# Optimization experiments

Hardware: AMD Instinct MI355X
Metric: run time of the kernel (lower is better)

The kernel has to match this reference:

```python
import jax, jax.numpy as jnp
import numpy as np

N = 50000      # nodes
E = 800000     # directed edges
GNN_DIM = 128  # node feature dim
HID = 64       # per-head hidden dim of conv1
HEADS = 2
OUT = 16       # output_dim (classes)
TEXT = 500     # tf-idf text dim
M = 10000      # masked / labeled nodes


def setup_inputs() -> dict:
    key = jax.random.key(0)
    ks = jax.random.split(key, 32)
    w = lambda k, s: jax.random.normal(k, s, jnp.float32) * 0.05
    inp = {
        'text_features': jax.random.normal(ks[0], (M, TEXT), jnp.float32),
        'x': jax.random.normal(ks[1], (N, GNN_DIM), jnp.float32),
        'edge_index': jax.random.randint(ks[2], (2, E), 0, N),
        'mask': jax.random.randint(ks[3], (M,), 0, N),
        # text MLP (Linear stored as [in, out])
        'fc1_w': w(ks[4], (TEXT, 128)), 'fc1_b': w(ks[5], (128,)),
        'fc2_w': w(ks[6], (128, 64)),  'fc2_b': w(ks[7], (64,)),
        'fc3_w': w(ks[8], (64, 16)),   'fc3_b': w(ks[9], (16,)),
        'fc4_w': w(ks[10], (16, OUT)), 'fc4_b': w(ks[11], (OUT,)),
        'sc_w': w(ks[12], (TEXT, OUT)), 'sc_b': w(ks[13], (OUT,)),
        # GATConv1: in=GNN_DIM, heads=2, out=HID, concat=True
        'W1': w(ks[14], (GNN_DIM, HEADS * HID)),
        'att_src1': w(ks[15], (HEADS, HID)), 'att_dst1': w(ks[16], (HEADS, HID)),
        'b1': w(ks[17], (HEADS * HID,)),
        # GATConv2: in=2*HID, heads=1, out=OUT, concat=False
        'W2': w(ks[18], (HEADS * HID, OUT)),
        'att_src2': w(ks[19], (1, OUT)), 'att_dst2': w(ks[20], (1, OUT)),
        'b2': w(ks[21], (OUT,)),
        # fc_final: [2*OUT, OUT]
        'fcf_w': w(ks[22], (2 * OUT, OUT)), 'fcf_b': w(ks[23], (OUT,)),
    }
    return inp


def _gat_layer(h_in, src, dst, W, a_src, a_dst, b, heads, dim, concat):
    # PyG GATConv (default negative_slope=0.2, self-loops already appended)
    n = h_in.shape[0]
    h = (h_in @ W).reshape(n, heads, dim)                      # [N,H,D]
    a_s = jnp.einsum('nhd,hd->nh', h, a_src)                   # [N,H]
    a_d = jnp.einsum('nhd,hd->nh', h, a_dst)
    e = jax.nn.leaky_relu(a_s[src] + a_d[dst], 0.2)            # [E,H]
    emax = jax.ops.segment_max(e, dst, num_segments=n)
    ex = jnp.exp(e - emax[dst])
    den = jax.ops.segment_sum(ex, dst, num_segments=n)
    alpha = ex / (den[dst] + 1e-16)                            # [E,H]
    msg = h[src] * alpha[:, :, None]                           # [E,H,D]
    out = jax.ops.segment_sum(msg, dst, num_segments=n)        # [N,H,D]
    out = out.reshape(n, heads * dim) if concat else out.mean(axis=1)
    return out + b


def reference(text_features, x, edge_index, mask,
              fc1_w, fc1_b, fc2_w, fc2_b, fc3_w, fc3_b, fc4_w, fc4_b,
              sc_w, sc_b, W1, att_src1, att_dst1, b1,
              W2, att_src2, att_dst2, b2, fcf_w, fcf_b):
    n = x.shape[0]
    loop = jnp.arange(n, dtype=edge_index.dtype)
    src = jnp.concatenate([edge_index[0], loop])
    dst = jnp.concatenate([edge_index[1], loop])

    # GNN branch
    g = jax.nn.relu(_gat_layer(x, src, dst, W1, att_src1, att_dst1, b1,
                               HEADS, HID, True))
    g = _gat_layer(g, src, dst, W2, att_src2, att_dst2, b2, 1, OUT, False)
    gnn_out = g[mask]                                          # [M,OUT]

    # text MLP branch with shortcut
    t = jax.nn.relu(text_features @ fc1_w + fc1_b)
    t = jax.nn.relu(t @ fc2_w + fc2_b)
    t = jax.nn.relu(t @ fc3_w + fc3_b)
    text_out = (t @ fc4_w + fc4_b) + (text_features @ sc_w + sc_b)  # [M,OUT]

    combined = jnp.concatenate([text_out, gnn_out], axis=1)    # [M,2*OUT]
    return jax.nn.log_softmax(combined @ fcf_w + fcf_b, axis=1)
```

## Files before the change

### kernel.cpp

```cpp
#include <hip/hip_runtime.h>
#include <hip/hip_bf16.h>
#include <cmath>

#define TEXTD 500
#define GNN_DIM 128
#define DEGP(v) ((v) << 5)

typedef __attribute__((ext_vector_type(8))) short bf16x8;
typedef __attribute__((ext_vector_type(4))) float f32x4;

__device__ __forceinline__ float bf2f(unsigned short u) {
    union { unsigned int i; float f; } cv;
    cv.i = ((unsigned int)u) << 16;
    return cv.f;
}
__device__ __forceinline__ unsigned short f2b(float x) {
    __hip_bfloat16 b = __float2bfloat16(x);
    return *reinterpret_cast<unsigned short*>(&b);
}
__device__ __forceinline__ float u2f(unsigned int u) {
    union { unsigned int i; float f; } cv; cv.i = u; return cv.f;
}
__device__ __forceinline__ bf16x8 cvt8(const float* p) {
    float4 u = *(const float4*)p;
    float4 v = *(const float4*)(p + 4);
    bf16x8 f;
    f[0] = (short)f2b(u.x); f[1] = (short)f2b(u.y);
    f[2] = (short)f2b(u.z); f[3] = (short)f2b(u.w);
    f[4] = (short)f2b(v.x); f[5] = (short)f2b(v.y);
    f[6] = (short)f2b(v.z); f[7] = (short)f2b(v.w);
    return f;
}

__global__ __launch_bounds__(256) void setup_kernel(
    int* __restrict__ deg, int N, int NB,
    const float* __restrict__ fc1_w, const float* __restrict__ sc_w,
    const float* __restrict__ W1, const float* __restrict__ W2,
    const float* __restrict__ fc2_w, const float* __restrict__ fc3_w,
    const float* __restrict__ fc4_w,
    unsigned short* __restrict__ w1cat, unsigned short* __restrict__ w1g,
    unsigned short* __restrict__ w2t, unsigned short* __restrict__ fc2t,
    unsigned short* __restrict__ fc3t, unsigned short* __restrict__ fc4t)
{
    if ((int)blockIdx.x < NB) {
        int v = blockIdx.x * 256 + threadIdx.x;
        if (v < N) deg[DEGP(v)] = 0;
        return;
    }
    int idx = (blockIdx.x - NB) * 256 + threadIdx.x;
    if (idx < 73728) {
        int n = idx >> 9, k = idx & 511;
        float v = 0.f;
        if (k < TEXTD) v = (n < 128) ? fc1_w[k * 128 + n] : sc_w[k * 16 + (n - 128)];
        w1cat[idx] = f2b(v);
    } else if (idx < 90112) {
        int j = idx - 73728;
        int n = j >> 7, k = j & 127;
        w1g[j] = f2b(W1[k * 128 + n]);
    } else if (idx < 92160) {
        int j = idx - 90112;
        int n = j >> 7, k = j & 127;
        w2t[j] = f2b(W2[k * 16 + n]);
    } else if (idx < 100352) {
        int j = idx - 92160;
        int n = j >> 7, k = j & 127;
        fc2t[j] = f2b(fc2_w[k * 64 + n]);
    } else if (idx < 101376) {
        int j = idx - 100352;
        int n = j >> 6, k = j & 63;
        fc3t[j] = f2b(fc3_w[k * 16 + n]);
    } else if (idx < 101888) {
        int j = idx - 101376;
        int n = j >> 5, k = j & 31;
        fc4t[j] = f2b((k < 16) ? fc4_w[k * 16 + n] : 0.f);
    }
}

__global__ __launch_bounds__(256) void text_mfma_kernel(
    const float* __restrict__ text, const short* __restrict__ w1cat,
    const float* __restrict__ fc1_b, const float* __restrict__ sc_b,
    const short* __restrict__ fc2t, const float* __restrict__ fc2_b,
    const short* __restrict__ fc3t, const float* __restrict__ fc3_b,
    const short* __restrict__ fc4t, const float* __restrict__ fc4_b,
    float* __restrict__ text_out, int M)
{
    __shared__ float part[4 * 9 * 256];
    __shared__ unsigned short t1b[16 * 136];
    __shared__ unsigned short t2b[16 * 72];
    __shared__ unsigned short t3b[16 * 40];
    __shared__ float tscs[16 * 16];

    const int tid = threadIdx.x;
    const int w = tid >> 6, lane = tid & 63;
    const int q = lane >> 4, col = lane & 15;
    const int mb = blockIdx.x * 16;
    const int arow = min(mb + col, M - 1);
    const int kofs = w * 128;

    bf16x8 afrag[4];
    #pragma unroll
    for (int ks = 0; ks < 4; ks++) {
        int k0 = kofs + ks * 32 + q * 8;
        if (k0 + 7 < TEXTD) {
            afrag[ks] = cvt8(text + (size_t)arow * TEXTD + k0);
        } else {
            bf16x8 f;
            #pragma unroll
            for (int e = 0; e < 8; e++) {
                int k = k0 + e;
                f[e] = (short)((k < TEXTD) ? f2b(text[(size_t)arow * TEXTD + k]) : 0);
            }
            afrag[ks] = f;
        }
    }

    for (int nb = 0; nb < 9; nb++) {
        const short* bp = w1cat + (size_t)(nb * 16 + col) * 512 + kofs + q * 8;
        f32x4 acc = {0.f, 0.f, 0.f, 0.f};
        #pragma unroll
        for (int ks = 0; ks < 4; ks++)
            acc = __builtin_amdgcn_mfma_f32_16x16x32_bf16(afrag[ks], *(const bf16x8*)(bp + ks * 32), acc, 0, 0, 0);
        #pragma unroll
        for (int i = 0; i < 4; i++)
            part[w * 2304 + nb * 256 + i * 64 + lane] = acc[i];
    }
    __syncthreads();

    {
        int nb0 = w * 2;
        int cnt = (w == 3) ? 3 : 2;
        for (int t = 0; t < cnt; t++) {
            int nb = nb0 + t;
            #pragma unroll
            for (int i = 0; i < 4; i++) {
                float a = part[nb * 256 + i * 64 + lane]
                        + part[2304 + nb * 256 + i * 64 + lane]
                        + part[4608 + nb * 256 + i * 64 + lane]
                        + part[6912 + nb * 256 + i * 64 + lane];
                int row = q * 4 + i;
                if (nb < 8) t1b[row * 136 + nb * 16 + col] = f2b(fmaxf(a + fc1_b[nb * 16 + col], 0.f));
                else        tscs[row * 16 + col] = a + sc_b[col];
            }
        }
    }
    __syncthreads();

    {
        const unsigned short* a2p = t1b + col * 136 + q * 8;
        const short* bp = fc2t + (w * 16 + col) * 128 + q * 8;
        f32x4 acc = {0.f, 0.f, 0.f, 0.f};
        #pragma unroll
        for (int ks = 0; ks < 4; ks++)
            acc = __builtin_amdgcn_mfma_f32_16x16x32_bf16(
                *(const bf16x8*)(a2p + ks * 32), *(const bf16x8*)(bp + ks * 32), acc, 0, 0, 0);
        #pragma unroll
        for (int i = 0; i < 4; i++) {
            int row = q * 4 + i;
            t2b[row * 72 + w * 16 + col] = f2b(fmaxf(acc[i] + fc2_b[w * 16 + col], 0.f));
        }
    }
    __syncthreads();

    if (w == 0) {
        {
            const unsigned short* a3p = t2b + col * 72 + q * 8;
            const short* bp = fc3t + col * 64 + q * 8;
            f32x4 acc = {0.f, 0.f, 0.f, 0.f};
            #pragma unroll
            for (int ks = 0; ks < 2; ks++)
                acc = __builtin_amdgcn_mfma_f32_16x16x32_bf16(
                    *(const bf16x8*)(a3p + ks * 32), *(const bf16x8*)(bp + ks * 32), acc, 0, 0, 0);
            #pragma unroll
            for (int i = 0; i < 4; i++) {
                int row = q * 4 + i;
                t3b[row * 40 + col] = f2b(fmaxf(acc[i] + fc3_b[col], 0.f));
                t3b[row * 40 + 16 + col] = 0;
            }
        }
        {
            const unsigned short* a4p = t3b + col * 40 + q * 8;
            const short* bp = fc4t + col * 32 + q * 8;
            f32x4 acc = {0.f, 0.f, 0.f, 0.f};
            acc = __builtin_amdgcn_mfma_f32_16x16x32_bf16(
                *(const bf16x8*)a4p, *(const bf16x8*)bp, acc, 0, 0, 0);
            #pragma unroll
            for (int i = 0; i < 4; i++) {
                int row = q * 4 + i;
                int rg = mb + row;
                if (rg < M) text_out[(size_t)rg * 16 + col] = acc[i] + fc4_b[col] + tscs[row * 16 + col];
            }
        }
    }
}

__global__ __launch_bounds__(256) void gemm_h1_kernel(
    const float* __restrict__ x, const short* __restrict__ B,
    const float* __restrict__ as1w, const float* __restrict__ ad1w,
    unsigned short* __restrict__ h1, float* __restrict__ a_s, float* __restrict__ a_d, int N)
{
    const int tid = threadIdx.x;
    const int wave = tid >> 6, lane = tid & 63;
    const int q = lane >> 4, col = lane & 15;
    const int mb = blockIdx.x * 64 + wave * 16;
    const int arow = min(mb + col, N - 1);
    const float* ap = x + (size_t)arow * 128 + q * 8;

    bf16x8 afrag[4];
    #pragma unroll
    for (int ks = 0; ks < 4; ks++) afrag[ks] = cvt8(ap + ks * 32);

    float ps0[4] = {0,0,0,0}, ps1[4] = {0,0,0,0};
    float pd0[4] = {0,0,0,0}, pd1[4] = {0,0,0,0};

    #pragma unroll
    for (int nb = 0; nb < 8; nb++) {
        const short* bp = B + (size_t)(nb * 16 + col) * 128 + q * 8;
        f32x4 acc = {0.f, 0.f, 0.f, 0.f};
        #pragma unroll
        for (int ks = 0; ks < 4; ks++)
            acc = __builtin_amdgcn_mfma_f32_16x16x32_bf16(afrag[ks], *(const bf16x8*)(bp + ks * 32), acc, 0, 0, 0);
        const int j = nb * 16 + col;
        const float asj = as1w[j], adj = ad1w[j];
        #pragma unroll
        for (int i = 0; i < 4; i++) {
            int row = mb + q * 4 + i;
            if (row < N) h1[(size_t)row * 128 + j] = f2b(acc[i]);
            if (nb < 4) { ps0[i] = fmaf(acc[i], asj, ps0[i]); pd0[i] = fmaf(acc[i], adj, pd0[i]); }
            else        { ps1[i] = fmaf(acc[i], asj, ps1[i]); pd1[i] = fmaf(acc[i], adj, pd1[i]); }
        }
    }
    #pragma unroll
    for (int i = 0; i < 4; i++) {
        float v0 = ps0[i], v1 = ps1[i], w0 = pd0[i], w1 = pd1[i];
        #pragma unroll
        for (int off = 1; off < 16; off <<= 1) {
            v0 += __shfl_xor(v0, off, 16);
            v1 += __shfl_xor(v1, off, 16);
            w0 += __shfl_xor(w0, off, 16);
            w1 += __shfl_xor(w1, off, 16);
        }
        int row = mb + q * 4 + i;
        if (col == 0 && row < N) {
            a_s[2 * row] = v0; a_s[2 * row + 1] = v1;
            a_d[2 * row] = w0; a_d[2 * row + 1] = w1;
        }
    }
}

__global__ __launch_bounds__(256) void deg_hist_kernel(
    const int* __restrict__ edst, int* __restrict__ deg, int* __restrict__ rank, int E)
{
    const int base = blockIdx.x * 1024 + threadIdx.x;
    int e0 = base;
    int e1 = base + 256;
    int e2 = base + 512;
    int e3 = base + 768;
    int d0 = (e0 < E) ? edst[e0] : -1;
    int d1 = (e1 < E) ? edst[e1] : -1;
    int d2 = (e2 < E) ? edst[e2] : -1;
    int d3 = (e3 < E) ? edst[e3] : -1;
    int r0 = (d0 >= 0) ? atomicAdd(&deg[DEGP(d0)], 1) : 0;
    int r1 = (d1 >= 0) ? atomicAdd(&deg[DEGP(d1)], 1) : 0;
    int r2 = (d2 >= 0) ? atomicAdd(&deg[DEGP(d2)], 1) : 0;
    int r3 = (d3 >= 0) ? atomicAdd(&deg[DEGP(d3)], 1) : 0;
    if (d0 >= 0) rank[e0] = r0;
    if (d1 >= 0) rank[e1] = r1;
    if (d2 >= 0) rank[e2] = r2;
    if (d3 >= 0) rank[e3] = r3;
}

__global__ __launch_bounds__(256) void part_kernel(
    const int* __restrict__ deg, int* __restrict__ bsum, int N)
{
    const int tid = threadIdx.x;
    int i = blockIdx.x * 256 + tid;
    int d = (i < N) ? deg[DEGP(i)] + 1 : 0;
    #pragma unroll
    for (int off = 32; off > 0; off >>= 1) d += __shfl_down(d, off, 64);
    __shared__ int wsum[4];
    if ((tid & 63) == 0) wsum[tid >> 6] = d;
    __syncthreads();
    if (tid == 0) bsum[blockIdx.x] = wsum[0] + wsum[1] + wsum[2] + wsum[3];
}

__global__ __launch_bounds__(256) void rowptr_kernel(
    const int* __restrict__ deg, const int* __restrict__ bsum,
    int* __restrict__ rowptr, int N, int NB)
{
    __shared__ int bsc[256];
    __shared__ int sc[256];
    const int tid = threadIdx.x;

    int bv = (tid < NB) ? bsum[tid] : 0;
    bsc[tid] = bv;
    for (int off = 1; off < 256; off <<= 1) {
        __syncthreads();
        int t = (tid >= off) ? bsc[tid - off] : 0;
        __syncthreads();
        bsc[tid] += t;
    }
    __syncthreads();
    const int base = (blockIdx.x == 0) ? 0 : bsc[blockIdx.x - 1];

    const int i = blockIdx.x * 256 + tid;
    int d = (i < N) ? deg[DEGP(i)] + 1 : 0;
    sc[tid] = d;
    for (int off = 1; off < 256; off <<= 1) {
        __syncthreads();
        int t = (tid >= off) ? sc[tid - off] : 0;
        __syncthreads();
        sc[tid] += t;
    }
    __syncthreads();
    int incl = sc[tid];
    if (i < N) rowptr[i] = base + incl - d;
    if (i == N - 1) rowptr[N] = base + incl;
}

__device__ __forceinline__ float edge_w(float e) {
    return __expf(e > 0.f ? e : 0.2f * e);
}

__global__ __launch_bounds__(256) void fillw_kernel(
    const int* __restrict__ esrc, const int* __restrict__ edst,
    const int* __restrict__ rank, const int* __restrict__ rowptr,
    uint2* __restrict__ eslot,
    const float* __restrict__ a_s, const float* __restrict__ a_d, int E, int N)
{
    int e = blockIdx.x * 256 + threadIdx.x;
    if (e < E) {
        int src = esrc[e], dst = edst[e];
        int pos = rowptr[dst] + 1 + rank[e];
        float2 as = *(const float2*)(a_s + 2 * src);
        float2 ad = *(const float2*)(a_d + 2 * dst);
        unsigned int w0 = f2b(edge_w(as.x + ad.x));
        unsigned int w1 = f2b(edge_w(as.y + ad.y));
        uint2 o; o.x = (unsigned int)src; o.y = (w1 << 16) | w0;
        eslot[pos] = o;
    } else if (e < E + N) {
        int v = e - E;
        float2 as = *(const float2*)(a_s + 2 * v);
        float2 ad = *(const float2*)(a_d + 2 * v);
        unsigned int w0 = f2b(edge_w(as.x + ad.x));
        unsigned int w1 = f2b(edge_w(as.y + ad.y));
        uint2 o; o.x = (unsigned int)v; o.y = (w1 << 16) | w0;
        eslot[rowptr[v]] = o;
    }
}

template<int B>
__device__ __forceinline__ void gat1_batch(
    int i0, int end, int endm1, int wsh,
    const uint2* __restrict__ eslot, const uint2* __restrict__ h1u, unsigned int dp,
    float& a0, float& a1, float& a2, float& a3, float& den)
{
    int ics[B];
    uint2 sl[B];
    float wv[B];
    uint2 hv[B];
    #pragma unroll
    for (int k = 0; k < B; k++) ics[k] = min(i0 + 2 * k, endm1);
    #pragma unroll
    for (int k = 0; k < B; k++) sl[k] = eslot[ics[k]];
    #pragma unroll
    for (int k = 0; k < B; k++) {
        float w = u2f((sl[k].y << wsh) & 0xffff0000u);
        wv[k] = (i0 + 2 * k < end) ? w : 0.f;
    }
    #pragma unroll
    for (int k = 0; k < B; k++) hv[k] = h1u[(sl[k].x << 5) | dp];
    #pragma unroll
    for (int k = 0; k < B; k++) {
        float w = wv[k];
        den += w;
        a0 = fmaf(w, u2f(hv[k].x << 16),          a0);
        a1 = fmaf(w, u2f(hv[k].x & 0xffff0000u),  a1);
        a2 = fmaf(w, u2f(hv[k].y << 16),          a2);
        a3 = fmaf(w, u2f(hv[k].y & 0xffff0000u),  a3);
    }
}

__global__ __launch_bounds__(256) void gat1_gather_kernel(
    const int* __restrict__ rowptr, const uint2* __restrict__ eslot,
    const uint2* __restrict__ h1u,
    const float* __restrict__ b1, uint2* __restrict__ g1b, int N)
{
    const int v = blockIdx.x * 4 + (threadIdx.x >> 6);
    if (v >= N) return;
    const int lane = threadIdx.x & 63;
    const int slot = lane >> 5;
    const unsigned int dp = lane & 31;
    const int head = dp >> 4;
    const int wsh = head ? 0 : 16;
    const int beg = rowptr[v], end = rowptr[v + 1];
    const int deg = end - beg;
    const int endm1 = end - 1;
    const int i0 = beg + slot;

    float a0 = 0.f, a1 = 0.f, a2 = 0.f, a3 = 0.f, den = 0.f;

    if (deg <= 8) {
        gat1_batch<4>(i0, end, endm1, wsh, eslot, h1u, dp, a0, a1, a2, a3, den);
    } else {
        gat1_batch<8>(i0, end, endm1, wsh, eslot, h1u, dp, a0, a1, a2, a3, den);
        for (int base = i0 + 16; base < end; base += 8)
            gat1_batch<4>(base, end, endm1, wsh, eslot, h1u, dp, a0, a1, a2, a3, den);
    }

    a0 += __shfl_xor(a0, 32, 64);
    a1 += __shfl_xor(a1, 32, 64);
    a2 += __shfl_xor(a2, 32, 64);
    a3 += __shfl_xor(a3, 32, 64);
    den += __shfl_xor(den, 32, 64);

    if (lane < 32) {
        float inv = 1.f / (den + 1e-16f);
        float4 bv = *(const float4*)(b1 + 4 * dp);
        float o0 = fmaxf(fmaf(a0, inv, bv.x), 0.f);
        float o1 = fmaxf(fmaf(a1, inv, bv.y), 0.f);
        float o2 = fmaxf(fmaf(a2, inv, bv.z), 0.f);
        float o3 = fmaxf(fmaf(a3, inv, bv.w), 0.f);
        uint2 o;
        o.x = ((unsigned int)f2b(o1) << 16) | f2b(o0);
        o.y = ((unsigned int)f2b(o3) << 16) | f2b(o2);
        g1b[((unsigned int)v << 5) | dp] = o;
    }
}

__global__ __launch_bounds__(256) void gat2_proj_kernel(
    const unsigned short* __restrict__ g1b, const short* __restrict__ w2t,
    const float* __restrict__ as2w, const float* __restrict__ ad2w,
    float* __restrict__ h2, float* __restrict__ a_s2, float* __restrict__ a_d2, int N)
{
    const int tid = threadIdx.x;
    const int wave = tid >> 6, lane = tid & 63;
    const int q = lane >> 4, col = lane & 15;
    const int mb = blockIdx.x * 64 + wave * 16;
    const int arow = min(mb + col, N - 1);
    const short* ap = (const short*)g1b + (size_t)arow * 128 + q * 8;
    const short* bp = w2t + (size_t)col * 128 + q * 8;

    f32x4 acc = {0.f, 0.f, 0.f, 0.f};
    #pragma unroll
    for (int ks = 0; ks < 4; ks++)
        acc = __builtin_amdgcn_mfma_f32_16x16x32_bf16(
            *(const bf16x8*)(ap + ks * 32), *(const bf16x8*)(bp + ks * 32), acc, 0, 0, 0);

    const float asj = as2w[col], adj = ad2w[col];
    #pragma unroll
    for (int i = 0; i < 4; i++) {
        int row = mb + q * 4 + i;
        float ps = acc[i] * asj, pd = acc[i] * adj;
        #pragma unroll
        for (int off = 1; off < 16; off <<= 1) {
            ps += __shfl_xor(ps, off, 16);
            pd += __shfl_xor(pd, off, 16);
        }
        if (row < N) {
            h2[(size_t)row * 16 + col] = acc[i];
            if (col == 0) { a_s2[row] = ps; a_d2[row] = pd; }
        }
    }
}

__global__ __launch_bounds__(256) void gat2_final_kernel(
    const int* __restrict__ rowptr, const uint2* __restrict__ eslot,
    const float* __restrict__ h2,
    const float* __restrict__ a_s2, const float* __restrict__ a_d2,
    const float* __restrict__ b2, const int* __restrict__ mask,
    const float* __restrict__ text_out,
    const float* __restrict__ fcf_w, const float* __restrict__ fcf_b,
    float* __restrict__ out, int M)
{
    const int tid = threadIdx.x;
    const int m = blockIdx.x * 4 + (tid >> 6);
    if (m >= M) return;
    const int lane = tid & 63, slot = lane >> 4, c = lane & 15;
    const int v = mask[m];
    const float adv = a_d2[v];
    const int beg = rowptr[v], end = rowptr[v + 1];
    const int i0 = beg + slot;

    float acc = 0.f, den = 0.f;
    unsigned int idxs[8];
    float msk[8], as_[8], hval[8];
    #pragma unroll
    for (int k = 0; k < 8; k++) {
        int i = i0 + 4 * k;
        int ic = min(i, end - 1);
        idxs[k] = eslot[ic].x;
        msk[k] = (i < end) ? 1.f : 0.f;
    }
    #pragma unroll
    for (int k = 0; k < 8; k++) as_[k] = a_s2[idxs[k]];
    #pragma unroll
    for (int k = 0; k < 8; k++) hval[k] = h2[(idxs[k] << 4) | (unsigned)c];
    #pragma unroll
    for (int k = 0; k < 8; k++) {
        float e = as_[k] + adv;
        float w = msk[k] * __expf(e > 0.f ? e : 0.2f * e);
        den += w;
        acc = fmaf(w, hval[k], acc);
    }
    for (int i = i0 + 32; i < end; i += 4) {
        unsigned int src = eslot[i].x;
        float e = a_s2[src] + adv;
        float w = __expf(e > 0.f ? e : 0.2f * e);
        den += w;
        acc = fmaf(w, h2[(src << 4) | (unsigned)c], acc);
    }

    acc += __shfl_xor(acc, 16, 64);
    acc += __shfl_xor(acc, 32, 64);
    den += __shfl_xor(den, 16, 64);
    den += __shfl_xor(den, 32, 64);

    if (slot == 0) {
        float gval = acc / (den + 1e-16f) + b2[c];
        float tval = text_out[(size_t)m * 16 + c];

        float logit = fcf_b[c];
        #pragma unroll
        for (int k = 0; k < 16; k++) {
            logit = fmaf(__shfl(tval, k, 16), fcf_w[k * 16 + c], logit);
            logit = fmaf(__shfl(gval, k, 16), fcf_w[(16 + k) * 16 + c], logit);
        }
        float mx = logit;
        #pragma unroll
        for (int off = 8; off > 0; off >>= 1) mx = fmaxf(mx, __shfl_xor(mx, off, 16));
        float se = expf(logit - mx);
        #pragma unroll
        for (int off = 8; off > 0; off >>= 1) se += __shfl_xor(se, off, 16);
        out[(size_t)m * 16 + c] = logit - mx - logf(se);
    }
}

extern "C" void kernel_launch(void* const* d_in, const int* in_sizes, int n_in,
                              void* d_out, int out_size, void* d_ws, size_t ws_size,
                              hipStream_t stream)
{
    const float* text  = (const float*)d_in[0];
    const float* x     = (const float*)d_in[1];
    const int*   ei    = (const int*)  d_in[2];
    const int*   mask  = (const int*)  d_in[3];
    const float* fc1_w = (const float*)d_in[4];  const float* fc1_b = (const float*)d_in[5];
    const float* fc2_w = (const float*)d_in[6];  const float* fc2_b = (const float*)d_in[7];
    const float* fc3_w = (const float*)d_in[8];  const float* fc3_b = (const float*)d_in[9];
    const float* fc4_w = (const float*)d_in[10]; const float* fc4_b = (const float*)d_in[11];
    const float* sc_w  = (const float*)d_in[12]; const float* sc_b  = (const float*)d_in[13];
    const float* W1    = (const float*)d_in[14];
    const float* as1w  = (const float*)d_in[15]; const float* ad1w  = (const float*)d_in[16];
    const float* b1    = (const float*)d_in[17];
    const float* W2    = (const float*)d_in[18];
    const float* as2w  = (const float*)d_in[19]; const float* ad2w  = (const float*)d_in[20];
    const float* b2    = (const float*)d_in[21];
    const float* fcf_w = (const float*)d_in[22]; const float* fcf_b = (const float*)d_in[23];

    const int M  = in_sizes[3];
    const int N  = in_sizes[1] / GNN_DIM;
    const int E  = in_sizes[2] / 2;
    const int EP = E + N;
    const int* esrc = ei;
    const int* edst = ei + E;

    const int Np = ((N + 63) / 64) * 64;
    const int NB = (N + 255) / 256;

    float* ws = (float*)d_ws;
    size_t off = 0;
    auto alloc = [&](size_t n) { float* p = ws + off; off += (n + 63) & ~size_t(63); return p; };

    unsigned short* h1    = (unsigned short*)alloc((size_t)Np * 64);
    unsigned int*   g1b   = (unsigned int*)  alloc((size_t)N * 64);
    unsigned short* w1cat = (unsigned short*)alloc(144 * 256);
    unsigned short* w1g   = (unsigned short*)alloc(128 * 64);
    unsigned short* w2t   = (unsigned short*)alloc(16 * 64);
    unsigned short* fc2t  = (unsigned short*)alloc(64 * 64);
    unsigned short* fc3t  = (unsigned short*)alloc(16 * 32);
    unsigned short* fc4t  = (unsigned short*)alloc(16 * 16);
    float* a_s1     = alloc((size_t)2 * N);
    float* a_d1     = alloc((size_t)2 * N);
    float* h2       = alloc((size_t)N * 16);
    float* a_s2     = alloc(N);
    float* a_d2     = alloc(N);
    float* text_out = alloc((size_t)M * 16);
    uint2* eslot    = (uint2*)alloc((size_t)2 * EP);
    int* deg        = (int*)alloc((size_t)N * 32);
    int* rank       = (int*)alloc(E);
    int* rowptr     = (int*)alloc(N + 1);
    int* bsum       = (int*)alloc(256);

    const int convBlocks = (101888 + 255) / 256;

    setup_kernel<<<NB + convBlocks, 256, 0, stream>>>(
        deg, N, NB, fc1_w, sc_w, W1, W2, fc2_w, fc3_w, fc4_w,
        w1cat, w1g, w2t, fc2t, fc3t, fc4t);

    deg_hist_kernel<<<(E + 1023) / 1024, 256, 0, stream>>>(edst, deg, rank, E);
    part_kernel<<<NB, 256, 0, stream>>>(deg, bsum, N);
    rowptr_kernel<<<NB, 256, 0, stream>>>(deg, bsum, rowptr, N, NB);

    gemm_h1_kernel<<<Np / 64, 256, 0, stream>>>(
        x, (const short*)w1g, as1w, ad1w, h1, a_s1, a_d1, N);

    fillw_kernel<<<(E + N + 255) / 256, 256, 0, stream>>>(
        esrc, edst, rank, rowptr, eslot, a_s1, a_d1, E, N);

    text_mfma_kernel<<<(M + 15) / 16, 256, 0, stream>>>(
        text, (const short*)w1cat, fc1_b, sc_b,
        (const short*)fc2t, fc2_b, (const short*)fc3t, fc3_b,
        (const short*)fc4t, fc4_b, text_out, M);

    gat1_gather_kernel<<<(N + 3) / 4, 256, 0, stream>>>(
        rowptr, eslot, (const uint2*)h1, b1, (uint2*)g1b, N);

    gat2_proj_kernel<<<Np / 64, 256, 0, stream>>>(
        (const unsigned short*)g1b, (const short*)w2t, as2w, ad2w, h2, a_s2, a_d2, N);

    gat2_final_kernel<<<(M + 3) / 4, 256, 0, stream>>>(
        rowptr, eslot, h2, a_s2, a_d2, b2, mask, text_out, fcf_w, fcf_b,
        (float*)d_out, M);
}
```

Baseline: 164.9 us.

## Fuse GAT layer-1 gather with layer-2 projection via shared-memory tile

Merges the layer-1 neighbor aggregation and the layer-2 MFMA projection into one kernel. Each 1024-thread block aggregates 16 nodes into a padded LDS tile, then one wave runs the 16x16 bf16 MFMA to produce h2 and the attention scalars. This drops the g1b round-trip through global memory and one kernel launch. In exchange, block size grows to 1024 and a __syncthreads is added, so waves that finish their gather early sit idle while the slowest node in the block is aggregated.

```diff
diff --git a/kernel.cpp b/kernel.cpp
--- a/kernel.cpp
+++ b/kernel.cpp
@@ -380,31 +380,40 @@
     }
 }
 
-__global__ __launch_bounds__(256) void gat1_gather_kernel(
+__global__ __launch_bounds__(1024) void gat1_fused_kernel(
     const int* __restrict__ rowptr, const uint2* __restrict__ eslot,
-    const uint2* __restrict__ h1u,
-    const float* __restrict__ b1, uint2* __restrict__ g1b, int N)
-{
-    const int v = blockIdx.x * 4 + (threadIdx.x >> 6);
-    if (v >= N) return;
-    const int lane = threadIdx.x & 63;
+    const uint2* __restrict__ h1u, const float* __restrict__ b1,
+    const short* __restrict__ w2t,
+    const float* __restrict__ as2w, const float* __restrict__ ad2w,
+    float* __restrict__ h2, float* __restrict__ a_s2, float* __restrict__ a_d2, int N)
+{
+    __shared__ unsigned short g1s[16 * 136];
+
+    const int tid = threadIdx.x;
+    const int w = tid >> 6, lane = tid & 63;
+    const int v = blockIdx.x * 16 + w;
+    const bool active = (v < N);
     const int slot = lane >> 5;
     const unsigned int dp = lane & 31;
     const int head = dp >> 4;
     const int wsh = head ? 0 : 16;
-    const int beg = rowptr[v], end = rowptr[v + 1];
+
+    int beg = 0, end = 0;
+    if (active) { beg = rowptr[v]; end = rowptr[v + 1]; }
     const int deg = end - beg;
     const int endm1 = end - 1;
     const int i0 = beg + slot;
 
     float a0 = 0.f, a1 = 0.f, a2 = 0.f, a3 = 0.f, den = 0.f;
 
-    if (deg <= 8) {
-        gat1_batch<4>(i0, end, endm1, wsh, eslot, h1u, dp, a0, a1, a2, a3, den);
-    } else {
-        gat1_batch<8>(i0, end, endm1, wsh, eslot, h1u, dp, a0, a1, a2, a3, den);
-        for (int base = i0 + 16; base < end; base += 8)
-            gat1_batch<4>(base, end, endm1, wsh, eslot, h1u, dp, a0, a1, a2, a3, den);
+    if (active) {
+        if (deg <= 8) {
+            gat1_batch<4>(i0, end, endm1, wsh, eslot, h1u, dp, a0, a1, a2, a3, den);
+        } else {
+            gat1_batch<8>(i0, end, endm1, wsh, eslot, h1u, dp, a0, a1, a2, a3, den);
+            for (int base = i0 + 16; base < end; base += 8)
+                gat1_batch<4>(base, end, endm1, wsh, eslot, h1u, dp, a0, a1, a2, a3, den);
+        }
     }
 
     a0 += __shfl_xor(a0, 32, 64);
@@ -414,51 +423,48 @@
     den += __shfl_xor(den, 32, 64);
 
     if (lane < 32) {
-        float inv = 1.f / (den + 1e-16f);
-        float4 bv = *(const float4*)(b1 + 4 * dp);
-        float o0 = fmaxf(fmaf(a0, inv, bv.x), 0.f);
-        float o1 = fmaxf(fmaf(a1, inv, bv.y), 0.f);
-        float o2 = fmaxf(fmaf(a2, inv, bv.z), 0.f);
-        float o3 = fmaxf(fmaf(a3, inv, bv.w), 0.f);
         uint2 o;
-        o.x = ((unsigned int)f2b(o1) << 16) | f2b(o0);
-        o.y = ((unsigned int)f2b(o3) << 16) | f2b(o2);
-        g1b[((unsigned int)v << 5) | dp] = o;
-    }
-}
-
-__global__ __launch_bounds__(256) void gat2_proj_kernel(
-    const unsigned short* __restrict__ g1b, const short* __restrict__ w2t,
-    const float* __restrict__ as2w, const float* __restrict__ ad2w,
-    float* __restrict__ h2, float* __restrict__ a_s2, float* __restrict__ a_d2, int N)
-{
-    const int tid = threadIdx.x;
-    const int wave = tid >> 6, lane = tid & 63;
-    const int q = lane >> 4, col = lane & 15;
-    const int mb = blockIdx.x * 64 + wave * 16;
-    const int arow = min(mb + col, N - 1);
-    const short* ap = (const short*)g1b + (size_t)arow * 128 + q * 8;
-    const short* bp = w2t + (size_t)col * 128 + q * 8;
-
-    f32x4 acc = {0.f, 0.f, 0.f, 0.f};
-    #pragma unroll
-    for (int ks = 0; ks < 4; ks++)
-        acc = __builtin_amdgcn_mfma_f32_16x16x32_bf16(
-            *(const bf16x8*)(ap + ks * 32), *(const bf16x8*)(bp + ks * 32), acc, 0, 0, 0);
-
-    const float asj = as2w[col], adj = ad2w[col];
-    #pragma unroll
-    for (int i = 0; i < 4; i++) {
-        int row = mb + q * 4 + i;
-        float ps = acc[i] * asj, pd = acc[i] * adj;
-        #pragma unroll
-        for (int off = 1; off < 16; off <<= 1) {
-            ps += __shfl_xor(ps, off, 16);
-            pd += __shfl_xor(pd, off, 16);
-        }
-        if (row < N) {
-            h2[(size_t)row * 16 + col] = acc[i];
-            if (col == 0) { a_s2[row] = ps; a_d2[row] = pd; }
+        if (active) {
+            float inv = 1.f / (den + 1e-16f);
+            float4 bv = *(const float4*)(b1 + 4 * dp);
+            float o0 = fmaxf(fmaf(a0, inv, bv.x), 0.f);
+            float o1 = fmaxf(fmaf(a1, inv, bv.y), 0.f);
+            float o2 = fmaxf(fmaf(a2, inv, bv.z), 0.f);
+            float o3 = fmaxf(fmaf(a3, inv, bv.w), 0.f);
+            o.x = ((unsigned int)f2b(o1) << 16) | f2b(o0);
+            o.y = ((unsigned int)f2b(o3) << 16) | f2b(o2);
+        } else {
+            o.x = 0; o.y = 0;
+        }
+        *(uint2*)&g1s[w * 136 + 4 * dp] = o;
+    }
+    __syncthreads();
+
+    if (w == 0) {
+        const int q = lane >> 4, col = lane & 15;
+        const unsigned short* ap = g1s + col * 136 + q * 8;
+        const short* bp = w2t + col * 128 + q * 8;
+
+        f32x4 acc = {0.f, 0.f, 0.f, 0.f};
+        #pragma unroll
+        for (int ks = 0; ks < 4; ks++)
+            acc = __builtin_amdgcn_mfma_f32_16x16x32_bf16(
+                *(const bf16x8*)(ap + ks * 32), *(const bf16x8*)(bp + ks * 32), acc, 0, 0, 0);
+
+        const float asj = as2w[col], adj = ad2w[col];
+        #pragma unroll
+        for (int i = 0; i < 4; i++) {
+            int vv = blockIdx.x * 16 + q * 4 + i;
+            float ps = acc[i] * asj, pd = acc[i] * adj;
+            #pragma unroll
+            for (int off = 1; off < 16; off <<= 1) {
+                ps += __shfl_xor(ps, off, 16);
+                pd += __shfl_xor(pd, off, 16);
+            }
+            if (vv < N) {
+                h2[(size_t)vv * 16 + col] = acc[i];
+                if (col == 0) { a_s2[vv] = ps; a_d2[vv] = pd; }
+            }
         }
     }
 }
@@ -571,7 +577,6 @@
     auto alloc = [&](size_t n) { float* p = ws + off; off += (n + 63) & ~size_t(63); return p; };
 
     unsigned short* h1    = (unsigned short*)alloc((size_t)Np * 64);
-    unsigned int*   g1b   = (unsigned int*)  alloc((size_t)N * 64);
     unsigned short* w1cat = (unsigned short*)alloc(144 * 256);
     unsigned short* w1g   = (unsigned short*)alloc(128 * 64);
     unsigned short* w2t   = (unsigned short*)alloc(16 * 64);
@@ -611,11 +616,9 @@
         (const short*)fc2t, fc2_b, (const short*)fc3t, fc3_b,
         (const short*)fc4t, fc4_b, text_out, M);
 
-    gat1_gather_kernel<<<(N + 3) / 4, 256, 0, stream>>>(
-        rowptr, eslot, (const uint2*)h1, b1, (uint2*)g1b, N);
-
-    gat2_proj_kernel<<<Np / 64, 256, 0, stream>>>(
-        (const unsigned short*)g1b, (const short*)w2t, as2w, ad2w, h2, a_s2, a_d2, N);
+    gat1_fused_kernel<<<(N + 15) / 16, 1024, 0, stream>>>(
+        rowptr, eslot, (const uint2*)h1, b1, (const short*)w2t,
+        as2w, ad2w, h2, a_s2, a_d2, N);
 
     gat2_final_kernel<<<(M + 3) / 4, 256, 0, stream>>>(
         rowptr, eslot, h2, a_s2, a_d2, b2, mask, text_out, fcf_w, fcf_b,
```

After: 166.8 us. Within noise of the previous version (+1.1%).
